# Performance work log

Hardware: AMD Instinct MI355X
Metric: run time of the kernel (lower is better)

The kernel has to match this reference:

```python
import jax
import jax.numpy as jnp
import numpy as np
from jax import lax


def _extrema_mask(x):
    # x: (W,). Mirrors the torch diff/pad/sign logic exactly.
    dx = x[1:] - x[:-1]
    right = jnp.pad(dx, (0, 1)) > 0          # F.pad(dx,[0,1]) > 0
    left = jnp.pad(dx, (1, 0)) <= 0          # F.pad(dx,[1,0]) <= 0
    s = (1 - jnp.sign(x)).astype(bool)       # True where x <= 0
    valleys = right & left & s
    peaks = (~right) & (~left) & (~s)
    return peaks | valleys


def _suppress_one(x, dist):
    # x: (W,) single signal. Greedy NMS-like suppression over extrema
    # sorted by |value| descending.
    W = x.shape[0]
    e = _extrema_mask(x)
    key = jnp.where(e, jnp.abs(x), -jnp.inf)  # non-extrema sort last
    order = jnp.argsort(-key)                 # descending by |x| among extrema
    pos = order                               # original positions, sorted
    valid = e[order]                          # padded (non-extrema) entries

    def step(is_sec, i):
        act = valid[i] & (~is_sec[i])
        within = (pos >= pos[i] - dist) & (pos <= pos[i] + dist)
        new = jnp.where(act, is_sec | within, is_sec)
        new = new.at[i].set(jnp.where(act, False, new[i]))
        return new, None

    is_sec, _ = lax.scan(step, jnp.zeros(W, dtype=bool), jnp.arange(W))
    primary = valid & (~is_sec)
    # pos is a permutation of 0..W-1, so scatter-set is exact
    out = jnp.zeros_like(x).at[pos].set(jnp.where(primary, x[pos], 0.0))
    return out


def setup_inputs() -> dict:
    key = jax.random.key(0)
    x = jax.random.normal(key, (128, 1, 4096), dtype=jnp.float32)
    return {"x": x, "minimum_extrema_distance": 32}


def reference(x, minimum_extrema_distance):
    B, C, W = x.shape  # C == 1 as assumed by the original module
    flat = x.reshape(B * C, W)
    out = jax.vmap(lambda s: _suppress_one(s, minimum_extrema_distance))(flat)
    return out.reshape(B, C, W)
```

## Files before the change

kernel.cpp:

```cpp
#include <hip/hip_runtime.h>

typedef unsigned long long u64;
typedef unsigned int u32;

#define W    4096
#define NT   128
#define CH   32
#define NCH  128
#define D32  32
#define RSTR 33
#define ROWS (NCH + 4)
#define PSI(b,a,cc,o) ((((b)*2+(a))*ROWS + ((cc)+2))*RSTR + (o))
#define HMI(b,cc)     ((b)*ROWS + ((cc)+2))

__global__ __launch_bounds__(NT) void extrema_nms_db(
    const float* __restrict__ x,
    const int*   __restrict__ dist_p,
    float*       __restrict__ out)
{
    const int sig = blockIdx.x;
    const float* xg = x + (size_t)sig * W;
    float*       og = out + (size_t)sig * W;
    const int dist = *dist_p;
    const int tid  = threadIdx.x;

    __shared__ __align__(16) u32 PS[4 * ROWS * RSTR];
    __shared__ u64 HM[2 * ROWS];
    __shared__ int LF;

    if (dist == D32) {
        const int base = tid * CH;

        for (int k = tid; k < 4 * 4 * RSTR; k += NT) {
            const int grp = k / (4 * RSTR);
            const int rem = k % (4 * RSTR);
            const int prw = rem / RSTR;
            const int oo  = rem % RSTR;
            const int cc  = (prw < 2) ? (prw - 2) : (NCH + prw - 2);
            PS[PSI(grp >> 1, grp & 1, cc, oo)] = 0u;
        }
        if (tid < 2) {
            HM[HMI(0, tid - 2)] = 0ull; HM[HMI(0, NCH + tid)] = 0ull;
            HM[HMI(1, tid - 2)] = 0ull; HM[HMI(1, NCH + tid)] = 0ull;
        }

        float f[CH + 2];
        {
            const float4* xg4 = (const float4*)xg + tid * 8;
            #pragma unroll
            for (int v = 0; v < 8; ++v) {
                const float4 q = xg4[v];
                f[4*v+1] = q.x; f[4*v+2] = q.y; f[4*v+3] = q.z; f[4*v+4] = q.w;
            }
            f[0]      = (tid > 0)      ? xg[base - 1]  : __int_as_float(0x7f800000);
            f[CH + 1] = (tid < NT - 1) ? xg[base + CH] : f[CH];
        }
        u32 kb[CH];
        #pragma unroll
        for (int j = 0; j < CH; ++j) {
            const float xi = f[j + 1];
            const bool right = f[j + 2] > xi;
            const bool left  = xi <= f[j];
            const bool s     = xi <= 0.0f;
            const bool ext   = (right && left && s) || (!right && !left && !s);
            const u32 ab = __float_as_uint(xi) & 0x7fffffffu;
            kb[j] = ext ? ((ab << 1) | 1u) : 0u;
        }
        u32 P = 0;
        #pragma unroll
        for (int j = 0; j < CH; ++j) if (kb[j]) P |= 1u << j;
        u32 best = 0; int bo = 0;
        #pragma unroll
        for (int j = 0; j < CH; ++j) if (kb[j] > best) { best = kb[j]; bo = j; }

        auto publish = [&](int b) {
            u32 a = 0;
            #pragma unroll
            for (int j = 0; j < CH; ++j) {
                const u32 kj = ((P >> j) & 1u) ? kb[j] : 0u;
                a = kj > a ? kj : a;
                PS[PSI(b, 0, tid, j)] = a;
            }
            a = 0;
            #pragma unroll
            for (int j = CH - 1; j >= 0; --j) {
                const u32 kj = ((P >> j) & 1u) ? kb[j] : 0u;
                a = kj > a ? kj : a;
                PS[PSI(b, 1, tid, j)] = a;
            }
            HM[HMI(b, tid)] = best ? (((u64)best << 32) | (u32)(base + bo)) : 0ull;
        };
        publish(0); publish(1);
        {
            const u64 bal = __ballot(P != 0u);
            if ((tid & 63) == 0 && bal) LF = 1;
        }
        int  kpos = -1;
        bool chgPrev = false;

        for (int r = 1;; ++r) {
            __syncthreads();
            const int pb = (r - 1) & 1;
            const int lf = LF;
            const u64 hL = HM[HMI(pb, tid - 1)];
            const u64 hR = HM[HMI(pb, tid + 1)];
            u32 sl = 0, pr = 0;
            if (P) {
                sl = PS[PSI(pb, 1, tid - 1, bo)];
                pr = PS[PSI(pb, 0, tid + 1, bo)];
            }
            if (lf != r) break;

            bool chg = false;
            if (P) {
                const bool keep_c = (sl < best) && (pr <= best);
                const u32 ML = (u32)(hL >> 32); const int pL = (int)(u32)hL;
                const u32 MR = (u32)(hR >> 32); const int pR = (int)(u32)hR;
                bool keep_m = false, keep_p = false;
                if (ML) {
                    const int boL = pL + D32 - base;
                    const u32 sl2 = PS[PSI(pb, 1, tid - 2, boL)];
                    const u32 pr2 = PS[PSI(pb, 0, tid,     boL)];
                    keep_m = (sl2 < ML) && (pr2 <= ML);
                }
                if (MR) {
                    const int boR = pR - D32 - base;
                    const u32 sl3 = PS[PSI(pb, 1, tid,     boR)];
                    const u32 pr3 = PS[PSI(pb, 0, tid + 2, boR)];
                    keep_p = (sl3 < MR) && (pr3 <= MR);
                }
                u32 newP = P;
                if (keep_m) {
                    const int e = pL + D32 - base;
                    newP &= (e >= 31) ? 0u : ~((1u << (e + 1)) - 1u);
                }
                if (keep_p) {
                    const int s2 = pR - D32 - base;
                    newP &= (s2 <= 0) ? 0u : ~(0xffffffffu << s2);
                }
                if (keep_c) { kpos = bo; newP = 0u; }
                if (newP != P) {
                    P = newP; chg = true;
                    if (!((P >> bo) & 1u)) {
                        best = 0; bo = 0;
                        #pragma unroll
                        for (int j = 0; j < CH; ++j) {
                            const u32 kj = ((P >> j) & 1u) ? kb[j] : 0u;
                            if (kj > best) { best = kj; bo = j; }
                        }
                    }
                }
            }
            if (chg || chgPrev) publish(r & 1);
            chgPrev = chg;
            const u64 bal = __ballot(P != 0u);
            if ((tid & 63) == 0 && bal) LF = r + 1;
        }

        {
            float4* og4 = (float4*)og + tid * 8;
            #pragma unroll
            for (int v = 0; v < 8; ++v) {
                const int j0 = 4 * v;
                float4 o;
                o.x = (kpos == j0    ) ? f[j0 + 1] : 0.0f;
                o.y = (kpos == j0 + 1) ? f[j0 + 2] : 0.0f;
                o.z = (kpos == j0 + 2) ? f[j0 + 3] : 0.0f;
                o.w = (kpos == j0 + 3) ? f[j0 + 4] : 0.0f;
                og4[v] = o;
            }
        }
    } else {
        u64* SK  = (u64*)PS;
        u64* red = HM;
        for (int i = tid; i < W; i += NT) og[i] = 0.0f;
        for (int i = tid; i < W; i += NT) {
            const float xi = xg[i];
            const bool right = (i < W - 1) ? (xg[i + 1] > xi) : false;
            const bool left  = (i > 0)     ? (xi <= xg[i - 1]) : true;
            const bool s = (xi <= 0.0f);
            const bool valley = right && left && s;
            const bool peak   = !right && !left && !s;
            const u32 ab = __float_as_uint(xi) & 0x7fffffffu;
            SK[i] = (valley || peak) ? (((u64)ab << 32) | (u64)(u32)(W - 1 - i)) : 0ull;
        }
        __syncthreads();

        for (;;) {
            u64 m = 0ull;
            #pragma unroll
            for (int j = 0; j < W / NT; ++j) {
                const u64 k = SK[tid + j * NT];
                if (k > m) m = k;
            }
            #pragma unroll
            for (int off = 32; off > 0; off >>= 1) {
                const u64 o = __shfl_down(m, off, 64);
                if (o > m) m = o;
            }
            if ((tid & 63) == 0) red[tid >> 6] = m;
            __syncthreads();
            if (tid == 0 && red[1] > red[0]) red[0] = red[1];
            __syncthreads();
            const u64 win = red[0];
            if (win == 0ull) break;

            const int p = (W - 1) - (int)(win & 0xffffffffu);
            if (tid == 0) og[p] = xg[p];

            int lo = p - dist; lo = lo < 0 ? 0 : lo;
            int hi = p + dist; hi = hi > (W - 1) ? (W - 1) : hi;
            for (int j = lo + tid; j <= hi; j += NT) SK[j] = 0ull;
            __syncthreads();
        }
    }
}

extern "C" void kernel_launch(void* const* d_in, const int* in_sizes, int n_in,
                              void* d_out, int out_size, void* d_ws, size_t ws_size,
                              hipStream_t stream) {
    const float* x      = (const float*)d_in[0];
    const int*   dist_p = (const int*)d_in[1];
    float*       out    = (float*)d_out;
    const int nsig = in_sizes[0] / W;
    hipLaunchKernelGGL(extrema_nms_db, dim3(nsig), dim3(NT), 0, stream,
                       x, dist_p, out);
}
```

Measured before the change: 17.78 us.

## Replace prefix/suffix max tables with kill-flag protocol for chunk NMS rounds

Drops the double-buffered prefix/suffix max arrays in shared memory that each chunk republished whenever its candidate set changed. Each round, every chunk now publishes only its best candidate, checks whether any of its own surviving extrema would beat a neighbour's best within range, and signals this through a per-chunk kill flag. A second barrier per round then lets each chunk decide which candidates are kept. This cuts the per-round shared-memory writes and table bookkeeping but doubles the barriers per round and adds 32-wide scans to compute the kill flags.

```diff
diff --git a/kernel.cpp b/kernel.cpp
--- a/kernel.cpp
+++ b/kernel.cpp
@@ -8,12 +8,8 @@
 #define CH   32
 #define NCH  128
 #define D32  32
-#define RSTR 33
-#define ROWS (NCH + 4)
-#define PSI(b,a,cc,o) ((((b)*2+(a))*ROWS + ((cc)+2))*RSTR + (o))
-#define HMI(b,cc)     ((b)*ROWS + ((cc)+2))
 
-__global__ __launch_bounds__(NT) void extrema_nms_db(
+__global__ __launch_bounds__(NT) void extrema_nms_r14(
     const float* __restrict__ x,
     const int*   __restrict__ dist_p,
     float*       __restrict__ out)
@@ -24,25 +20,13 @@
     const int dist = *dist_p;
     const int tid  = threadIdx.x;
 
-    __shared__ __align__(16) u32 PS[4 * ROWS * RSTR];
-    __shared__ u64 HM[2 * ROWS];
+    __shared__ u64 HM[NCH + 2];
+    __shared__ u32 KF[NCH + 2];
     __shared__ int LF;
+    __shared__ u64 SK[W];
 
     if (dist == D32) {
         const int base = tid * CH;
-
-        for (int k = tid; k < 4 * 4 * RSTR; k += NT) {
-            const int grp = k / (4 * RSTR);
-            const int rem = k % (4 * RSTR);
-            const int prw = rem / RSTR;
-            const int oo  = rem % RSTR;
-            const int cc  = (prw < 2) ? (prw - 2) : (NCH + prw - 2);
-            PS[PSI(grp >> 1, grp & 1, cc, oo)] = 0u;
-        }
-        if (tid < 2) {
-            HM[HMI(0, tid - 2)] = 0ull; HM[HMI(0, NCH + tid)] = 0ull;
-            HM[HMI(1, tid - 2)] = 0ull; HM[HMI(1, NCH + tid)] = 0ull;
-        }
 
         float f[CH + 2];
         {
@@ -63,8 +47,7 @@
             const bool left  = xi <= f[j];
             const bool s     = xi <= 0.0f;
             const bool ext   = (right && left && s) || (!right && !left && !s);
-            const u32 ab = __float_as_uint(xi) & 0x7fffffffu;
-            kb[j] = ext ? ((ab << 1) | 1u) : 0u;
+            kb[j] = ext ? (((__float_as_uint(xi) & 0x7fffffffu) << 1) | 1u) : 0u;
         }
         u32 P = 0;
         #pragma unroll
@@ -73,88 +56,73 @@
         #pragma unroll
         for (int j = 0; j < CH; ++j) if (kb[j] > best) { best = kb[j]; bo = j; }
 
-        auto publish = [&](int b) {
-            u32 a = 0;
-            #pragma unroll
-            for (int j = 0; j < CH; ++j) {
-                const u32 kj = ((P >> j) & 1u) ? kb[j] : 0u;
-                a = kj > a ? kj : a;
-                PS[PSI(b, 0, tid, j)] = a;
-            }
-            a = 0;
-            #pragma unroll
-            for (int j = CH - 1; j >= 0; --j) {
-                const u32 kj = ((P >> j) & 1u) ? kb[j] : 0u;
-                a = kj > a ? kj : a;
-                PS[PSI(b, 1, tid, j)] = a;
-            }
-            HM[HMI(b, tid)] = best ? (((u64)best << 32) | (u32)(base + bo)) : 0ull;
-        };
-        publish(0); publish(1);
-        {
-            const u64 bal = __ballot(P != 0u);
-            if ((tid & 63) == 0 && bal) LF = 1;
-        }
-        int  kpos = -1;
-        bool chgPrev = false;
+        if (tid < 2) { HM[tid * (NCH + 1)] = 0ull; KF[tid * (NCH + 1)] = 0u; }
+        KF[tid + 1] = 0u;
+        if (tid == 0) LF = 0;
 
+        int kpos = -1;
         for (int r = 1;; ++r) {
+            HM[tid + 1] = best ? (((u64)best << 32) | (u32)(base + bo)) : 0ull;
+            const u64 bal = __ballot(best != 0u);
+            if ((tid & 63) == 0 && bal) LF = r;
             __syncthreads();
-            const int pb = (r - 1) & 1;
             const int lf = LF;
-            const u64 hL = HM[HMI(pb, tid - 1)];
-            const u64 hR = HM[HMI(pb, tid + 1)];
-            u32 sl = 0, pr = 0;
-            if (P) {
-                sl = PS[PSI(pb, 1, tid - 1, bo)];
-                pr = PS[PSI(pb, 0, tid + 1, bo)];
-            }
+            const u64 hL = HM[tid];
+            const u64 hR = HM[tid + 2];
             if (lf != r) break;
 
-            bool chg = false;
-            if (P) {
-                const bool keep_c = (sl < best) && (pr <= best);
-                const u32 ML = (u32)(hL >> 32); const int pL = (int)(u32)hL;
-                const u32 MR = (u32)(hR >> 32); const int pR = (int)(u32)hR;
-                bool keep_m = false, keep_p = false;
-                if (ML) {
-                    const int boL = pL + D32 - base;
-                    const u32 sl2 = PS[PSI(pb, 1, tid - 2, boL)];
-                    const u32 pr2 = PS[PSI(pb, 0, tid,     boL)];
-                    keep_m = (sl2 < ML) && (pr2 <= ML);
-                }
-                if (MR) {
-                    const int boR = pR - D32 - base;
-                    const u32 sl3 = PS[PSI(pb, 1, tid,     boR)];
-                    const u32 pr3 = PS[PSI(pb, 0, tid + 2, boR)];
-                    keep_p = (sl3 < MR) && (pr3 <= MR);
-                }
-                u32 newP = P;
-                if (keep_m) {
-                    const int e = pL + D32 - base;
-                    newP &= (e >= 31) ? 0u : ~((1u << (e + 1)) - 1u);
-                }
-                if (keep_p) {
-                    const int s2 = pR - D32 - base;
-                    newP &= (s2 <= 0) ? 0u : ~(0xffffffffu << s2);
-                }
-                if (keep_c) { kpos = bo; newP = 0u; }
-                if (newP != P) {
-                    P = newP; chg = true;
-                    if (!((P >> bo) & 1u)) {
-                        best = 0; bo = 0;
+            const u32 ML = (u32)(hL >> 32); const int jm = (int)(u32)hL;
+            const u32 MR = (u32)(hR >> 32); const int jp = (int)(u32)hR;
+
+            if (ML && best > ML) {
+                const int e = jm + D32 - base;
+                u32 kill = 0;
+                #pragma unroll
+                for (int j = 0; j < CH; ++j)
+                    kill |= (j <= e && ((P >> j) & 1u) && kb[j] > ML) ? 1u : 0u;
+                if (kill) KF[tid] = (u32)r;
+            }
+            if (MR && best >= MR) {
+                const int s2 = jp - D32 - base;
+                u32 kill = 0;
+                #pragma unroll
+                for (int j = 0; j < CH; ++j)
+                    kill |= (j >= s2 && ((P >> j) & 1u) && kb[j] >= MR) ? 1u : 0u;
+                if (kill) KF[tid + 2] = (u32)r;
+            }
+            __syncthreads();
+            const u32 kfL = KF[tid];
+            const u32 kfC = KF[tid + 1];
+            const u32 kfR = KF[tid + 2];
+            const bool keep_m = ML && (kfL != (u32)r);
+            const bool keep_c = best && (kfC != (u32)r);
+            const bool keep_p = MR && (kfR != (u32)r);
+
+            u32 newP = P;
+            if (keep_m) { const int e  = jm + D32 - base;
+                          newP &= (e >= 31) ? 0u : ~((1u << (e + 1)) - 1u); }
+            if (keep_p) { const int s2 = jp - D32 - base;
+                          newP &= (s2 <= 0) ? 0u : ~(0xffffffffu << s2); }
+            if (keep_c) { kpos = bo; newP = 0u; }
+            if (newP != P) {
+                P = newP;
+                if (!((P >> bo) & 1u)) {
+                    best = 0;
+                    #pragma unroll
+                    for (int j = 0; j < CH; ++j) {
+                        const u32 kj = ((P >> j) & 1u) ? kb[j] : 0u;
+                        best = kj > best ? kj : best;
+                    }
+                    bo = 0;
+                    if (best) {
                         #pragma unroll
-                        for (int j = 0; j < CH; ++j) {
+                        for (int j = CH - 1; j >= 0; --j) {
                             const u32 kj = ((P >> j) & 1u) ? kb[j] : 0u;
-                            if (kj > best) { best = kj; bo = j; }
+                            if (kj == best) bo = j;
                         }
                     }
                 }
             }
-            if (chg || chgPrev) publish(r & 1);
-            chgPrev = chg;
-            const u64 bal = __ballot(P != 0u);
-            if ((tid & 63) == 0 && bal) LF = r + 1;
         }
 
         {
@@ -171,8 +139,6 @@
             }
         }
     } else {
-        u64* SK  = (u64*)PS;
-        u64* red = HM;
         for (int i = tid; i < W; i += NT) og[i] = 0.0f;
         for (int i = tid; i < W; i += NT) {
             const float xi = xg[i];
@@ -198,11 +164,11 @@
                 const u64 o = __shfl_down(m, off, 64);
                 if (o > m) m = o;
             }
-            if ((tid & 63) == 0) red[tid >> 6] = m;
+            if ((tid & 63) == 0) HM[tid >> 6] = m;
             __syncthreads();
-            if (tid == 0 && red[1] > red[0]) red[0] = red[1];
+            if (tid == 0 && HM[1] > HM[0]) HM[0] = HM[1];
             __syncthreads();
-            const u64 win = red[0];
+            const u64 win = HM[0];
             if (win == 0ull) break;
 
             const int p = (W - 1) - (int)(win & 0xffffffffu);
@@ -223,6 +189,6 @@
     const int*   dist_p = (const int*)d_in[1];
     float*       out    = (float*)d_out;
     const int nsig = in_sizes[0] / W;
-    hipLaunchKernelGGL(extrema_nms_db, dim3(nsig), dim3(NT), 0, stream,
+    hipLaunchKernelGGL(extrema_nms_r14, dim3(nsig), dim3(NT), 0, stream,
                        x, dist_p, out);
 }
```

After: 21.01 us. 1.18x slower.
